# Performance work log

Measured on AMD Instinct MI355X. Metric: run time of the kernel, lower is better.

The kernel has to match this reference:

```python
import jax, jax.numpy as jnp
import numpy as np

NUM_BASES = 8
DEGREE = 3
KSIZE = 3
DOMAIN = (0.0, 1.0)


def bspline_basis(x, degree, knots):
    """Cox-de Boor recursion, vectorized over all elements of x.
    x: [...] float; knots: [num_bases + degree + 1].
    Returns basis values of shape [..., num_bases].
    (The original torch code evaluates this same recursion per-tap inside
    nested loops; here it is evaluated once, batched, with correct knot
    index bookkeeping. Uniform distinct knots -> no zero denominators.)
    """
    xe = x[..., None]  # [..., 1]
    # degree-0: indicator of each knot interval -> [..., L-1]
    B = ((knots[:-1] <= xe) & (xe < knots[1:])).astype(x.dtype)
    for d in range(1, degree + 1):
        left = (xe - knots[:-(d + 1)]) / (knots[d:-1] - knots[:-(d + 1)]) * B[..., :-1]
        right = (knots[d + 1:] - xe) / (knots[d + 1:] - knots[1:-d]) * B[..., 1:]
        B = left + right  # [..., L-d-1]
    return B  # [..., num_bases]


def setup_inputs() -> dict:
    key = jax.random.key(0)
    k1, k2 = jax.random.split(key)
    # inputs uniform in [0,1) so they lie inside the B-spline domain
    x = jax.random.uniform(k1, (16, 64, 64, 64), dtype=jnp.float32)
    # per-tap spline coefficients: [Cout, Cin, K, K, num_bases]
    coeff = jax.random.normal(k2, (64, 64, KSIZE, KSIZE, NUM_BASES), dtype=jnp.float32)
    return {"x": x, "coeff": coeff}


def reference(x, coeff):
    # normalize to domain (identity for domain=(0,1), kept for faithfulness)
    xn = (x - DOMAIN[0]) / (DOMAIN[1] - DOMAIN[0])
    knots = jnp.linspace(DOMAIN[0], DOMAIN[1], NUM_BASES + DEGREE + 1, dtype=x.dtype)
    # spline basis for every input element: [B, Cin, H, W, nb]
    phi = bspline_basis(xn, DEGREE, knots)
    Bn, Cin, H, W, nb = phi.shape
    Cout = coeff.shape[0]
    # The KAN conv  out[b,o,h,w] = sum_{j,k,l,m} phi[b,j,h+k,w+l,m]*coeff[o,j,k,l,m]
    # is exactly a VALID conv with Cin*nb input channels.
    phi_c = jnp.transpose(phi, (0, 1, 4, 2, 3)).reshape(Bn, Cin * nb, H, W)
    w = jnp.transpose(coeff, (0, 1, 4, 2, 3)).reshape(Cout, Cin * nb, KSIZE, KSIZE)
    out = jax.lax.conv_general_dilated(
        phi_c, w, window_strides=(1, 1), padding="VALID",
        dimension_numbers=("NCHW", "OIHW", "NCHW"))
    return out  # [B, Cout, H-K+1, W-K+1]
```

## Files before the change

### kernel.cpp

```cpp
#include <hip/hip_runtime.h>
#include <hip/hip_bf16.h>


typedef short v8s __attribute__((ext_vector_type(8)));
typedef float v4f __attribute__((ext_vector_type(4)));
typedef float v16f __attribute__((ext_vector_type(16)));
typedef unsigned long long u64;
typedef u64 v2u64 __attribute__((ext_vector_type(2)));

#define B_N   16
#define CIN   64
#define COUT  64
#define H_IN  64
#define W_IN  64
#define NB    8
#define HO    62
#define WO    62
#define JC    8
#define NCH   8

__device__ __forceinline__ ushort f2bf(float f) {
    uint xu = __float_as_uint(f);
    return (ushort)((xu + 0x7fffu + ((xu >> 16) & 1u)) >> 16);
}

__global__ void prep_coeff_kernel(const float* __restrict__ coeff, ushort* __restrict__ bt) {
    int n = blockIdx.x * 256 + threadIdx.x;
    if (n >= 294912) return;
    int m  = n & 7;
    int g2 = (n >> 3) & 1;
    int o  = (n >> 4) & 63;
    int jp = (n >> 10) & 3;
    int q  = n >> 12;
    int tap = q % 9;
    int jc  = q / 9;
    int j = jc * 8 + jp * 2 + g2;
    bt[n] = f2bf(coeff[((o * CIN + j) * 9 + tap) * 8 + m]);
}

#define MFMA32(a, b, c) __builtin_amdgcn_mfma_f32_32x32x16_bf16((a), (b), (c), 0, 0, 0)
#define MFMA16(a, b, c) __builtin_amdgcn_mfma_f32_16x16x32_bf16((a), (b), (c), 0, 0, 0)

__global__ __launch_bounds__(256, 4) void kan_conv_ks(
        const float* __restrict__ x, const ushort* __restrict__ cb,
        float* __restrict__ out) {
    const int h    = blockIdx.x;
    const int b    = blockIdx.y;
    const int tid  = threadIdx.x;
    const int lane = tid & 63;
    const int kh   = tid >> 6;
    const int l31  = lane & 31;
    const int g2   = lane >> 5;

    __shared__ __align__(16) char smraw[32768];
    ushort* phi = (ushort*)smraw;

    v16f acc[2][2];
    #pragma unroll
    for (int t = 0; t < 2; ++t) {
        acc[t][0] = (v16f)(0.f);
        acc[t][1] = (v16f)(0.f);
    }

    float xreg[6];
    auto xload = [&](int jcn) {
        #pragma unroll
        for (int it = 0; it < 6; ++it) {
            int n = it * 256 + tid;
            xreg[it] = x[((b * CIN + jcn * 8 + ((n >> 6) & 7)) * H_IN
                          + (h + (n >> 9))) * W_IN + (n & 63)];
        }
    };
    xload(0);

    const char* pBbase = smraw + (kh * 2 + g2) * 1024 + l31 * 16;
    const v8s*  cbv    = reinterpret_cast<const v8s*>(cb) + kh * 128 + l31 * 2 + g2;

    for (int jc = 0; jc < NCH; ++jc) {
        #pragma unroll
        for (int it = 0; it < 6; ++it) {
            int n = it * 256 + tid;
            float s_ = xreg[it] * 11.0f;
            int i0 = (int)s_;
            i0 = i0 < 0 ? 0 : (i0 > 10 ? 10 : i0);
            float u  = s_ - (float)i0;
            float um = 1.0f - u;
            float u2 = u * u, u3 = u2 * u;
            const float inv6 = 1.0f / 6.0f;
            float n0 = um * um * um * inv6;
            float n1 = (3.0f * u3 - 6.0f * u2 + 4.0f) * inv6;
            float n2 = (-3.0f * u3 + 3.0f * u2 + 3.0f * u + 1.0f) * inv6;
            float n3 = u3 * inv6;
            u64 V = (u64)f2bf(n0) | ((u64)f2bf(n1) << 16)
                  | ((u64)f2bf(n2) << 32) | ((u64)f2bf(n3) << 48);
            int bi = i0 - 3;
            u64 lo = bi < 0 ? (V >> (uint)(-16 * bi))
                   : bi < 4 ? (V << (uint)(16 * bi)) : 0ull;
            u64 hi = bi <= 0 ? 0ull
                   : bi < 4 ? (V >> (uint)(64 - 16 * bi))
                   : (V << (uint)(16 * bi - 64));
            v2u64 pk; pk[0] = lo; pk[1] = hi;
            *reinterpret_cast<v2u64*>(&phi[n << 3]) = pk;
        }
        if (jc + 1 < NCH) xload(jc + 1);
        __syncthreads();

        const v8s* pAc = cbv + jc * 4608;
        #pragma unroll
        for (int tap = 0; tap < 9; ++tap) {
            const int k  = tap / 3;
            const int lt = tap - k * 3;
            v8s a0 = pAc[tap * 512];
            v8s a1 = pAc[tap * 512 + 64];
            v8s b0 = *reinterpret_cast<const v8s*>(pBbase + k * 8192 + lt * 16);
            v8s b1 = *reinterpret_cast<const v8s*>(pBbase + k * 8192 + lt * 16 + 512);
            acc[0][0] = MFMA32(a0, b0, acc[0][0]);
            acc[0][1] = MFMA32(a0, b1, acc[0][1]);
            acc[1][0] = MFMA32(a1, b0, acc[1][0]);
            acc[1][1] = MFMA32(a1, b1, acc[1][1]);
        }
        __syncthreads();
    }

    float* red = (float*)smraw;
    auto wr_acc = [&](int slot) {
        #pragma unroll
        for (int t = 0; t < 4; ++t)
            #pragma unroll
            for (int q = 0; q < 4; ++q) {
                v4f v;
                #pragma unroll
                for (int z = 0; z < 4; ++z) v[z] = acc[t >> 1][t & 1][q * 4 + z];
                *reinterpret_cast<v4f*>(smraw + slot * 16384 + (t * 4 + q) * 1024 + lane * 16) = v;
            }
    };
    auto add_acc = [&](int slot) {
        #pragma unroll
        for (int t = 0; t < 4; ++t)
            #pragma unroll
            for (int q = 0; q < 4; ++q) {
                v4f v = *reinterpret_cast<const v4f*>(smraw + slot * 16384 + (t * 4 + q) * 1024 + lane * 16);
                #pragma unroll
                for (int z = 0; z < 4; ++z) acc[t >> 1][t & 1][q * 4 + z] += v[z];
            }
    };
    if (kh == 1) wr_acc(0);
    if (kh == 3) wr_acc(1);
    __syncthreads();
    if (kh == 0) add_acc(0);
    if (kh == 2) add_acc(1);
    __syncthreads();
    if (kh == 2) wr_acc(0);
    __syncthreads();
    if (kh == 0) {
        add_acc(0);
        #pragma unroll
        for (int ot = 0; ot < 2; ++ot)
            #pragma unroll
            for (int wf = 0; wf < 2; ++wf) {
                int w = wf * 32 + l31;
                if (w < WO) {
                    #pragma unroll
                    for (int reg = 0; reg < 16; ++reg) {
                        int o = ot * 32 + (reg & 3) + 8 * (reg >> 2) + 4 * g2;
                        out[((b * COUT + o) * HO + h) * WO + w] = acc[ot][wf][reg];
                    }
                }
            }
    }
    (void)red;
}

__global__ __launch_bounds__(256, 4) void kan_conv_fb(
        const float* __restrict__ x, const float* __restrict__ coeff_f,
        float* __restrict__ out) {
    const int h    = blockIdx.x;
    const int b    = blockIdx.y;
    const int tid  = threadIdx.x;
    const int lane = tid & 63;
    const int wv   = tid >> 6;
    const int g    = lane >> 4;
    const int l15  = lane & 15;
    const int obase = (wv >> 1) << 5;
    const int wbase = (wv & 1) << 5;

    __shared__ __align__(16) ushort phi_lds[3 * JC * W_IN * NB];
    __shared__ uint lut[72];
    if (tid < 72) {
        int tap = tid;
        int j  = tap / 9;
        int r9 = tap - j * 9;
        int kt = r9 / 3;
        int lt = r9 - kt * 3;
        lut[tap] = (uint)(((kt * JC + j) * W_IN) * NB) | ((uint)lt << 16)
                 | ((uint)j << 20) | ((uint)r9 << 24);
    }
    v4f acc00 = {0.f, 0.f, 0.f, 0.f};
    v4f acc01 = acc00, acc10 = acc00, acc11 = acc00;
    const int aoff = obase + l15;
    float xv[6];
    #pragma unroll
    for (int it = 0; it < 6; ++it) {
        int n = it * 256 + tid;
        xv[it] = x[((b * CIN + ((n >> 6) & 7)) * H_IN + (h + (n >> 9))) * W_IN + (n & 63)];
    }
    for (int jc = 0; jc < NCH; ++jc) {
        #pragma unroll
        for (int it = 0; it < 6; ++it) {
            int n = it * 256 + tid;
            float s  = xv[it] * 11.0f;
            int i0 = (int)s;
            i0 = i0 < 0 ? 0 : (i0 > 10 ? 10 : i0);
            float u  = s - (float)i0;
            float um = 1.0f - u;
            float u2 = u * u, u3 = u2 * u;
            const float inv6 = 1.0f / 6.0f;
            float n0 = um * um * um * inv6;
            float n1 = (3.0f * u3 - 6.0f * u2 + 4.0f) * inv6;
            float n2 = (-3.0f * u3 + 3.0f * u2 + 3.0f * u + 1.0f) * inv6;
            float n3 = u3 * inv6;
            u64 V = (u64)f2bf(n0) | ((u64)f2bf(n1) << 16)
                  | ((u64)f2bf(n2) << 32) | ((u64)f2bf(n3) << 48);
            int bi = i0 - 3;
            u64 lo = bi < 0 ? (V >> (uint)(-16 * bi))
                   : bi < 4 ? (V << (uint)(16 * bi)) : 0ull;
            u64 hi = bi <= 0 ? 0ull
                   : bi < 4 ? (V >> (uint)(64 - 16 * bi))
                   : (V << (uint)(16 * bi - 64));
            v2u64 pk; pk[0] = lo; pk[1] = hi;
            *reinterpret_cast<v2u64*>(&phi_lds[n << 3]) = pk;
        }
        if (jc + 1 < NCH) {
            int j0n = (jc + 1) * JC;
            #pragma unroll
            for (int it = 0; it < 6; ++it) {
                int n = it * 256 + tid;
                xv[it] = x[((b * CIN + j0n + ((n >> 6) & 7)) * H_IN + (h + (n >> 9))) * W_IN + (n & 63)];
            }
        }
        __syncthreads();
        const int j0 = jc * JC;
        #pragma unroll 6
        for (int kk = 0; kk < 18; ++kk) {
            int tap = (kk << 2) + g;
            uint e = lut[tap];
            int philoc = (int)(e & 0xffffu);
            int lt     = (int)((e >> 16) & 3u);
            int w0 = wbase + l15 + lt;
            int w1 = w0 + 16;
            w0 = w0 < 63 ? w0 : 63;
            w1 = w1 < 63 ? w1 : 63;
            v8s pb0 = *reinterpret_cast<const v8s*>(&phi_lds[philoc + (w0 << 3)]);
            v8s pb1 = *reinterpret_cast<const v8s*>(&phi_lds[philoc + (w1 << 3)]);
            int j  = (int)((e >> 20) & 15u);
            int r9 = (int)((e >> 24) & 15u);
            const float* cf = coeff_f + (((aoff * CIN + (j0 + j)) * 9 + r9) << 3);
            v8s pa0, pa1;
            #pragma unroll
            for (int z = 0; z < 8; ++z) pa0[z] = (short)f2bf(cf[z]);
            const float* cf2 = cf + (CIN * 9 * NB * 16);
            #pragma unroll
            for (int z = 0; z < 8; ++z) pa1[z] = (short)f2bf(cf2[z]);
            acc00 = MFMA16(pa0, pb0, acc00);
            acc01 = MFMA16(pa0, pb1, acc01);
            acc10 = MFMA16(pa1, pb0, acc10);
            acc11 = MFMA16(pa1, pb1, acc11);
        }
        __syncthreads();
    }
    const int wc0 = wbase + l15;
    const int wc1 = wc0 + 16;
    #pragma unroll
    for (int i = 0; i < 2; ++i) {
        v4f a0 = (i == 0) ? acc00 : acc10;
        v4f a1 = (i == 0) ? acc01 : acc11;
        int o = obase + i * 16 + (g << 2);
        #pragma unroll
        for (int r = 0; r < 4; ++r) {
            int off = ((b * COUT + o + r) * HO + h) * WO;
            if (wc0 < WO) out[off + wc0] = a0[r];
            if (wc1 < WO) out[off + wc1] = a1[r];
        }
    }
}

extern "C" void kernel_launch(void* const* d_in, const int* in_sizes, int n_in,
                              void* d_out, int out_size, void* d_ws, size_t ws_size,
                              hipStream_t stream) {
    const float* x     = (const float*)d_in[0];
    const float* coeff = (const float*)d_in[1];
    float* out = (float*)d_out;

    const size_t bt_bytes = (size_t)294912 * 2;
    if (ws_size >= bt_bytes) {
        ushort* bt = (ushort*)d_ws;
        prep_coeff_kernel<<<(294912 + 255) / 256, 256, 0, stream>>>(coeff, bt);
        kan_conv_ks<<<dim3(HO, B_N), 256, 0, stream>>>(x, bt, out);
    } else {
        kan_conv_fb<<<dim3(HO, B_N), 256, 0, stream>>>(x, coeff, out);
    }
}
```

Measured before the change: 56.18 us.

## Per-wave private phi slices with software-pipelined spline evaluation, no block barriers

Each wave now evaluates the B-spline basis only for the two input channels it consumes and writes them into its own LDS region. This removes the two __syncthreads per channel chunk in the main loop. The basis computation for the next chunk is interleaved between the MFMA taps of the current chunk, and x loads are prefetched two chunks ahead. The bf16 packing uses the v_cvt_pk_bf16_f32 instruction, and the final cross-wave reduction and global store are split across two waves. The cost is more live registers for the double-buffered x values, plus reliance on in-order LDS access within a wave when the buffer is overwritten.

```diff
diff --git a/kernel.cpp b/kernel.cpp
--- a/kernel.cpp
+++ b/kernel.cpp
@@ -22,6 +22,12 @@
 __device__ __forceinline__ ushort f2bf(float f) {
     uint xu = __float_as_uint(f);
     return (ushort)((xu + 0x7fffu + ((xu >> 16) & 1u)) >> 16);
+}
+
+__device__ __forceinline__ uint cvtpk(float a, float b) {
+    uint r;
+    asm("v_cvt_pk_bf16_f32 %0, %1, %2" : "=v"(r) : "v"(a), "v"(b));
+    return r;
 }
 
 __global__ void prep_coeff_kernel(const float* __restrict__ coeff, ushort* __restrict__ bt) {
@@ -41,7 +47,7 @@
 #define MFMA32(a, b, c) __builtin_amdgcn_mfma_f32_32x32x16_bf16((a), (b), (c), 0, 0, 0)
 #define MFMA16(a, b, c) __builtin_amdgcn_mfma_f32_16x16x32_bf16((a), (b), (c), 0, 0, 0)
 
-__global__ __launch_bounds__(256, 4) void kan_conv_ks(
+__global__ __launch_bounds__(256, 4) void kan_conv_ks2(
         const float* __restrict__ x, const ushort* __restrict__ cb,
         float* __restrict__ out) {
     const int h    = blockIdx.x;
@@ -53,77 +59,87 @@
     const int g2   = lane >> 5;
 
     __shared__ __align__(16) char smraw[32768];
-    ushort* phi = (ushort*)smraw;
+
+    char* wrB = smraw + kh * 6144 + lane * 16;
+    const char* rdB = smraw + kh * 6144 + g2 * 1024 + l31 * 16;
 
     v16f acc[2][2];
+    acc[0][0] = (v16f)(0.f); acc[0][1] = (v16f)(0.f);
+    acc[1][0] = (v16f)(0.f); acc[1][1] = (v16f)(0.f);
+
+    float xr[2][6];
+    const float* xb = x + ((size_t)(b * CIN) * H_IN + h) * W_IN + lane;
+    const int jx = kh * 2;
+
+    auto XL = [&](int dst, int jc) {
+        #pragma unroll
+        for (int e = 0; e < 6; ++e) {
+            int k = e >> 1, j2 = e & 1;
+            xr[dst][e] = xb[(size_t)(jc * 8 + jx + j2) * (H_IN * W_IN) + k * W_IN];
+        }
+    };
+    auto PW = [&](int src, int e) {
+        float s_ = xr[src][e] * 11.0f;
+        int i0 = (int)s_;
+        i0 = i0 < 0 ? 0 : (i0 > 10 ? 10 : i0);
+        float u  = s_ - (float)i0;
+        float um = 1.0f - u;
+        float u2 = u * u, u3 = u2 * u;
+        const float inv6 = 1.0f / 6.0f;
+        float n0 = um * um * um * inv6;
+        float n1 = (3.0f * u3 - 6.0f * u2 + 4.0f) * inv6;
+        float n2 = (-3.0f * u3 + 3.0f * u2 + 3.0f * u + 1.0f) * inv6;
+        float n3 = u3 * inv6;
+        u64 V = (u64)cvtpk(n0, n1) | ((u64)cvtpk(n2, n3) << 32);
+        int bi = i0 - 3;
+        u64 lo = bi < 0 ? (V >> (uint)(-16 * bi))
+               : bi < 4 ? (V << (uint)(16 * bi)) : 0ull;
+        u64 hi = bi <= 0 ? 0ull
+               : bi < 4 ? (V >> (uint)(64 - 16 * bi))
+               : (V << (uint)(16 * bi - 64));
+        v2u64 pk; pk[0] = lo; pk[1] = hi;
+        *reinterpret_cast<v2u64*>(wrB + e * 1024) = pk;
+    };
+    auto TAP = [&](const char* pAc, int k, int lt, int tap) {
+        v8s b0 = *reinterpret_cast<const v8s*>(rdB + k * 2048 + lt * 16);
+        v8s b1 = *reinterpret_cast<const v8s*>(rdB + k * 2048 + 512 + lt * 16);
+        v8s a0 = *reinterpret_cast<const v8s*>(pAc + tap * 8192);
+        v8s a1 = *reinterpret_cast<const v8s*>(pAc + tap * 8192 + 1024);
+        acc[0][0] = MFMA32(a0, b0, acc[0][0]);
+        acc[0][1] = MFMA32(a0, b1, acc[0][1]);
+        acc[1][0] = MFMA32(a1, b0, acc[1][0]);
+        acc[1][1] = MFMA32(a1, b1, acc[1][1]);
+    };
+
+    const char* pA = (const char*)cb + (size_t)(kh * 128 + l31 * 2 + g2) * 16;
+
+    XL(0, 0);
     #pragma unroll
-    for (int t = 0; t < 2; ++t) {
-        acc[t][0] = (v16f)(0.f);
-        acc[t][1] = (v16f)(0.f);
-    }
-
-    float xreg[6];
-    auto xload = [&](int jcn) {
-        #pragma unroll
-        for (int it = 0; it < 6; ++it) {
-            int n = it * 256 + tid;
-            xreg[it] = x[((b * CIN + jcn * 8 + ((n >> 6) & 7)) * H_IN
-                          + (h + (n >> 9))) * W_IN + (n & 63)];
-        }
-    };
-    xload(0);
-
-    const char* pBbase = smraw + (kh * 2 + g2) * 1024 + l31 * 16;
-    const v8s*  cbv    = reinterpret_cast<const v8s*>(cb) + kh * 128 + l31 * 2 + g2;
-
-    for (int jc = 0; jc < NCH; ++jc) {
-        #pragma unroll
-        for (int it = 0; it < 6; ++it) {
-            int n = it * 256 + tid;
-            float s_ = xreg[it] * 11.0f;
-            int i0 = (int)s_;
-            i0 = i0 < 0 ? 0 : (i0 > 10 ? 10 : i0);
-            float u  = s_ - (float)i0;
-            float um = 1.0f - u;
-            float u2 = u * u, u3 = u2 * u;
-            const float inv6 = 1.0f / 6.0f;
-            float n0 = um * um * um * inv6;
-            float n1 = (3.0f * u3 - 6.0f * u2 + 4.0f) * inv6;
-            float n2 = (-3.0f * u3 + 3.0f * u2 + 3.0f * u + 1.0f) * inv6;
-            float n3 = u3 * inv6;
-            u64 V = (u64)f2bf(n0) | ((u64)f2bf(n1) << 16)
-                  | ((u64)f2bf(n2) << 32) | ((u64)f2bf(n3) << 48);
-            int bi = i0 - 3;
-            u64 lo = bi < 0 ? (V >> (uint)(-16 * bi))
-                   : bi < 4 ? (V << (uint)(16 * bi)) : 0ull;
-            u64 hi = bi <= 0 ? 0ull
-                   : bi < 4 ? (V >> (uint)(64 - 16 * bi))
-                   : (V << (uint)(16 * bi - 64));
-            v2u64 pk; pk[0] = lo; pk[1] = hi;
-            *reinterpret_cast<v2u64*>(&phi[n << 3]) = pk;
-        }
-        if (jc + 1 < NCH) xload(jc + 1);
-        __syncthreads();
-
-        const v8s* pAc = cbv + jc * 4608;
-        #pragma unroll
-        for (int tap = 0; tap < 9; ++tap) {
-            const int k  = tap / 3;
-            const int lt = tap - k * 3;
-            v8s a0 = pAc[tap * 512];
-            v8s a1 = pAc[tap * 512 + 64];
-            v8s b0 = *reinterpret_cast<const v8s*>(pBbase + k * 8192 + lt * 16);
-            v8s b1 = *reinterpret_cast<const v8s*>(pBbase + k * 8192 + lt * 16 + 512);
-            acc[0][0] = MFMA32(a0, b0, acc[0][0]);
-            acc[0][1] = MFMA32(a0, b1, acc[0][1]);
-            acc[1][0] = MFMA32(a1, b0, acc[1][0]);
-            acc[1][1] = MFMA32(a1, b1, acc[1][1]);
-        }
-        __syncthreads();
-    }
-
-    float* red = (float*)smraw;
-    auto wr_acc = [&](int slot) {
+    for (int e = 0; e < 6; ++e) PW(0, e);
+    XL(1, 1);
+
+    auto CHUNK = [&](int jc, int cur, int nxt) {
+        const char* pAc = pA + (size_t)jc * 73728;
+        TAP(pAc, 0, 0, 0);
+        TAP(pAc, 0, 1, 1);
+        if (jc + 2 < NCH) XL(nxt, jc + 2);
+        TAP(pAc, 0, 2, 2);
+        if (jc + 1 < NCH) { PW(cur, 0); PW(cur, 1); }
+        TAP(pAc, 1, 0, 3);
+        TAP(pAc, 1, 1, 4);
+        TAP(pAc, 1, 2, 5);
+        if (jc + 1 < NCH) { PW(cur, 2); PW(cur, 3); }
+        TAP(pAc, 2, 0, 6);
+        TAP(pAc, 2, 1, 7);
+        TAP(pAc, 2, 2, 8);
+        if (jc + 1 < NCH) { PW(cur, 4); PW(cur, 5); }
+    };
+    for (int jj = 0; jj < 4; ++jj) {
+        CHUNK(2 * jj,     1, 0);
+        CHUNK(2 * jj + 1, 0, 1);
+    }
+
+    auto wr_full = [&](int off) {
         #pragma unroll
         for (int t = 0; t < 4; ++t)
             #pragma unroll
@@ -131,44 +147,68 @@
                 v4f v;
                 #pragma unroll
                 for (int z = 0; z < 4; ++z) v[z] = acc[t >> 1][t & 1][q * 4 + z];
-                *reinterpret_cast<v4f*>(smraw + slot * 16384 + (t * 4 + q) * 1024 + lane * 16) = v;
-            }
-    };
-    auto add_acc = [&](int slot) {
+                *reinterpret_cast<v4f*>(smraw + off + (t * 4 + q) * 1024 + lane * 16) = v;
+            }
+    };
+    auto add_full = [&](int off) {
         #pragma unroll
         for (int t = 0; t < 4; ++t)
             #pragma unroll
             for (int q = 0; q < 4; ++q) {
-                v4f v = *reinterpret_cast<const v4f*>(smraw + slot * 16384 + (t * 4 + q) * 1024 + lane * 16);
+                v4f v = *reinterpret_cast<const v4f*>(smraw + off + (t * 4 + q) * 1024 + lane * 16);
                 #pragma unroll
                 for (int z = 0; z < 4; ++z) acc[t >> 1][t & 1][q * 4 + z] += v[z];
             }
     };
-    if (kh == 1) wr_acc(0);
-    if (kh == 3) wr_acc(1);
+    auto wr_half = [&](int ot, int off) {
+        #pragma unroll
+        for (int wf = 0; wf < 2; ++wf)
+            #pragma unroll
+            for (int q = 0; q < 4; ++q) {
+                v4f v;
+                #pragma unroll
+                for (int z = 0; z < 4; ++z) v[z] = acc[ot][wf][q * 4 + z];
+                *reinterpret_cast<v4f*>(smraw + off + (wf * 4 + q) * 1024 + lane * 16) = v;
+            }
+    };
+    auto add_half = [&](int ot, int off) {
+        #pragma unroll
+        for (int wf = 0; wf < 2; ++wf)
+            #pragma unroll
+            for (int q = 0; q < 4; ++q) {
+                v4f v = *reinterpret_cast<const v4f*>(smraw + off + (wf * 4 + q) * 1024 + lane * 16);
+                #pragma unroll
+                for (int z = 0; z < 4; ++z) acc[ot][wf][q * 4 + z] += v[z];
+            }
+    };
+
     __syncthreads();
-    if (kh == 0) add_acc(0);
-    if (kh == 2) add_acc(1);
+    if (kh == 1) wr_full(0);
+    if (kh == 3) wr_full(16384);
     __syncthreads();
-    if (kh == 2) wr_acc(0);
+    if (kh == 0) add_full(0);
+    if (kh == 2) add_full(16384);
     __syncthreads();
-    if (kh == 0) {
-        add_acc(0);
-        #pragma unroll
-        for (int ot = 0; ot < 2; ++ot)
-            #pragma unroll
-            for (int wf = 0; wf < 2; ++wf) {
-                int w = wf * 32 + l31;
-                if (w < WO) {
-                    #pragma unroll
-                    for (int reg = 0; reg < 16; ++reg) {
-                        int o = ot * 32 + (reg & 3) + 8 * (reg >> 2) + 4 * g2;
-                        out[((b * COUT + o) * HO + h) * WO + w] = acc[ot][wf][reg];
-                    }
+    if (kh == 2) wr_half(0, 0);
+    if (kh == 0) wr_half(1, 8192);
+    __syncthreads();
+    if (kh == 0) add_half(0, 0);
+    if (kh == 2) add_half(1, 8192);
+
+    if (kh == 0 || kh == 2) {
+        const int ot = kh >> 1;
+        #pragma unroll
+        for (int wf = 0; wf < 2; ++wf) {
+            int w = wf * 32 + l31;
+            if (w < WO) {
+                #pragma unroll
+                for (int reg = 0; reg < 16; ++reg) {
+                    int o = ot * 32 + (reg & 3) + 8 * (reg >> 2) + 4 * g2;
+                    out[((b * COUT + o) * HO + h) * WO + w] = acc[ot][wf][reg];
                 }
             }
-    }
-    (void)red;
+        }
+    }
 }
 
 __global__ __launch_bounds__(256, 4) void kan_conv_fb(
@@ -295,7 +335,7 @@
     if (ws_size >= bt_bytes) {
         ushort* bt = (ushort*)d_ws;
         prep_coeff_kernel<<<(294912 + 255) / 256, 256, 0, stream>>>(coeff, bt);
-        kan_conv_ks<<<dim3(HO, B_N), 256, 0, stream>>>(x, bt, out);
+        kan_conv_ks2<<<dim3(HO, B_N), 256, 0, stream>>>(x, bt, out);
     } else {
         kan_conv_fb<<<dim3(HO, B_N), 256, 0, stream>>>(x, coeff, out);
     }
```

Result: slower. 77.27 us (+37.5%).
